# Optimization experiments

Measured on AMD Instinct MI355X. Metric: run time of the kernel, lower is better.

The kernel has to match this reference:

```python
import jax, jax.numpy as jnp
import numpy as np
import math

B, N, D_IN, D_OUT = 8, 2048, 128, 128
NEG_BIG = -10000.0

def setup_inputs() -> dict:
    key = jax.random.key(0)
    k_in, k_adj, kq, kk, kv, kbq, kbk, kbv = jax.random.split(key, 8)
    scale = 1.0 / math.sqrt(D_IN)
    inputs = jax.random.normal(k_in, (B, N, D_IN), dtype=jnp.float32)
    adj = jax.random.randint(k_adj, (B, N, N), 0, 2, dtype=jnp.int32)
    Wq = jax.random.uniform(kq, (D_IN, D_OUT), jnp.float32, -scale, scale)
    Wk = jax.random.uniform(kk, (D_IN, D_OUT), jnp.float32, -scale, scale)
    Wv = jax.random.uniform(kv, (D_IN, D_OUT), jnp.float32, -scale, scale)
    bq = jax.random.uniform(kbq, (D_OUT,), jnp.float32, -scale, scale)
    bk = jax.random.uniform(kbk, (D_OUT,), jnp.float32, -scale, scale)
    bv = jax.random.uniform(kbv, (D_OUT,), jnp.float32, -scale, scale)
    return {"inputs": inputs, "adj": adj, "Wq": Wq, "bq": bq,
            "Wk": Wk, "bk": bk, "Wv": Wv, "bv": bv}

def reference(inputs, adj, Wq, bq, Wk, bk, Wv, bv):
    # QKV projections: [B, N, D_OUT]
    q = inputs @ Wq + bq
    k = inputs @ Wk + bk
    v = inputs @ Wv + bv
    # additive adjacency bias: 0 where edge, -10000 where no edge
    bias = (1.0 - adj.astype(jnp.float32)) * NEG_BIG
    # scaled dot-product scores [B, N, N]
    a = jnp.einsum('bnd,bmd->bnm', q, k) / jnp.sqrt(jnp.float32(q.shape[-1]))
    a = a + bias
    p = jax.nn.softmax(a, axis=-1)  # dropout_prob=0.0 -> identity
    h = jnp.einsum('bnm,bmd->bnd', p, v)
    return jax.nn.elu(h)
```

## Files before the change

kernel.cpp:

```cpp
#include <hip/hip_runtime.h>

typedef unsigned short u16;
typedef unsigned int   u32;
typedef unsigned long long u64;
typedef __bf16 bf16x8 __attribute__((ext_vector_type(8)));
typedef float  fx4    __attribute__((ext_vector_type(4)));

__device__ __forceinline__ u16 f2bf(float f) {
    unsigned int x = __builtin_bit_cast(unsigned int, f);
    x = x + 0x7fffu + ((x >> 16) & 1u);
    return (u16)(x >> 16);
}
__device__ __forceinline__ __bf16 f2bf16(float f) {
    return __builtin_bit_cast(__bf16, f2bf(f));
}
__device__ __forceinline__ u16 f2bf_fast(float f) {
    return __builtin_bit_cast(u16, (__bf16)f);
}
__device__ __forceinline__ float exp2_fast(float x) {
#if __has_builtin(__builtin_amdgcn_exp2f)
    return __builtin_amdgcn_exp2f(x);
#else
    float r;
    __asm__ volatile("v_exp_f32 %0, %1" : "=v"(r) : "v"(x));
    return r;
#endif
}
__device__ __forceinline__ int ld_nt(const int* p) {
    return __builtin_nontemporal_load(p);
}

#define MFMA16(a, b, c) __builtin_amdgcn_mfma_f32_16x16x32_bf16((a), (b), (c), 0, 0, 0)
#define WAVE_LDS_SYNC() __asm__ volatile("s_waitcnt lgkmcnt(0)" ::: "memory")

__global__ __launch_bounds__(256) void wt_kernel(
    const float* __restrict__ Wq, const float* __restrict__ Wk,
    const float* __restrict__ Wv, u16* __restrict__ WT)
{
    const int o = blockIdx.x * 256 + threadIdx.x;
    const int p = o >> 14, rem = o & 16383, c = rem >> 7, k = rem & 127;
    const float* W = (p == 0) ? Wq : ((p == 1) ? Wk : Wv);
    WT[o] = f2bf(W[k * 128 + c]);
}

__global__ __launch_bounds__(256) void pack_kernel(
    const int* __restrict__ adj, u64* __restrict__ mask64)
{
    const int w = threadIdx.x >> 6, lane = threadIdx.x & 63;
    const int gw = blockIdx.x * 4 + w;
    const int nw = gridDim.x * 4;
    for (int it = gw; it < 131072; it += nw) {
        const int* base = adj + (size_t)it * 256 + lane;
        const u64 b0 = __ballot(ld_nt(base +   0) != 0);
        const u64 b1 = __ballot(ld_nt(base +  64) != 0);
        const u64 b2 = __ballot(ld_nt(base + 128) != 0);
        const u64 b3 = __ballot(ld_nt(base + 192) != 0);
        if (lane < 4) {
            const u64 v = (lane == 0) ? b0 : (lane == 1) ? b1 : (lane == 2) ? b2 : b3;
            mask64[(size_t)it * 4 + lane] = v;
        }
    }
}

__global__ __launch_bounds__(256, 2) void qkv_kernel(
    const float* __restrict__ X, const u16* __restrict__ WT,
    const float* __restrict__ bq, const float* __restrict__ bk,
    const float* __restrict__ bv,
    u16* __restrict__ Qf, u16* __restrict__ Kf, u16* __restrict__ Vf)
{
    __shared__ __align__(16) u16 st[4][1024];

    const int tid  = threadIdx.x;
    const int w    = tid >> 6;
    const int lane = tid & 63;
    const int n    = lane & 15;
    const int quad = lane >> 4;
    const int gw   = blockIdx.x * 4 + w;
    const int rt   = gw >> 1, ch = gw & 1;
    const int row0 = rt * 16;
    const int b    = row0 >> 11;
    const int keyb = row0 & 2047;

    u16* sw = st[w];

    bf16x8 af[4];
    {
        const float* xr = X + (size_t)(row0 + n) * 128;
#pragma unroll
        for (int kk = 0; kk < 4; ++kk) {
            float4 f0 = *(const float4*)(xr + kk * 32 + quad * 8);
            float4 f1 = *(const float4*)(xr + kk * 32 + quad * 8 + 4);
            bf16x8 a;
            a[0] = f2bf16(f0.x); a[1] = f2bf16(f0.y); a[2] = f2bf16(f0.z); a[3] = f2bf16(f0.w);
            a[4] = f2bf16(f1.x); a[5] = f2bf16(f1.y); a[6] = f2bf16(f1.z); a[7] = f2bf16(f1.w);
            af[kk] = a;
        }
    }

    const float* Bs[2] = {bq, bk};
#pragma unroll
    for (int p = 0; p < 2; ++p) {
        const u16* wt = WT + p * 16384;
#pragma unroll
        for (int nt = 0; nt < 4; ++nt) {
            const int col0 = ch * 64 + nt * 16;
            fx4 acc = {0.f, 0.f, 0.f, 0.f};
#pragma unroll
            for (int kk = 0; kk < 4; ++kk) {
                bf16x8 bf = __builtin_bit_cast(bf16x8,
                    *(const uint4*)&wt[(col0 + n) * 128 + kk * 32 + quad * 8]);
                acc = MFMA16(af[kk], bf, acc);
            }
            const float bb = Bs[p][col0 + n];
            const int c = col0 + n;
            const int li = ((c >> 5) & 1) * 512 + ((c >> 3) & 3) * 128 + (c & 7);
#pragma unroll
            for (int r = 0; r < 4; ++r)
                sw[li + (quad * 4 + r) * 8] = f2bf(acc[r] + bb);
        }
        WAVE_LDS_SYNC();
        u16* gbase;
        if (p == 0) {
            gbase = Qf + (((size_t)(b * 128 + (keyb >> 4)) * 4 + 2 * ch) << 9);
        } else {
            gbase = Kf + (((size_t)((b * 64 + (keyb >> 5)) * 2 + ((keyb >> 4) & 1)) * 4 + 2 * ch) << 9);
        }
        *(uint4*)(gbase + lane * 8)       = *(const uint4*)(sw + lane * 8);
        *(uint4*)(gbase + 512 + lane * 8) = *(const uint4*)(sw + 512 + lane * 8);
    }

    {
        const u16* wtv = WT + 2 * 16384;
        const int hk    = (keyb >> 4) & 1;
        const int vtile = keyb >> 5;
#pragma unroll
        for (int d0 = 0; d0 < 4; ++d0) {
            const int dbase = ch * 64 + d0 * 16;
            fx4 acc = {0.f, 0.f, 0.f, 0.f};
#pragma unroll
            for (int kk = 0; kk < 4; ++kk) {
                bf16x8 wf = __builtin_bit_cast(bf16x8,
                    *(const uint4*)&wtv[(dbase + n) * 128 + kk * 32 + quad * 8]);
                acc = MFMA16(wf, af[kk], acc);
            }
            const int li = d0 * 256 + ((n >> 3) & 1) * 128 + (n & 7);
#pragma unroll
            for (int r = 0; r < 4; ++r)
                sw[li + (quad * 4 + r) * 8] = f2bf(acc[r] + bv[dbase + quad * 4 + r]);
        }
        WAVE_LDS_SYNC();
        const int l5 = lane >> 5, lo = lane & 31;
#pragma unroll
        for (int i = 0; i < 2; ++i) {
            const int c2 = l5 + 2 * i;
            u16* g = Vf + (((size_t)(b * 64 + vtile) * 8 + ch * 4 + c2) << 9)
                        + hk * 256 + lo * 8;
            *(uint4*)g = *(const uint4*)(sw + c2 * 256 + lo * 8);
        }
    }
}

__global__ __launch_bounds__(256, 4) void attn_kernel(
    const u16* __restrict__ Qf, const u16* __restrict__ Kf,
    const u16* __restrict__ Vf, const u32* __restrict__ mask,
    float* __restrict__ out)
{
    __shared__ __align__(16) float mO[4][16 * 128];
    __shared__ __align__(16) float ml[4][16];
    __shared__ __align__(16) u16 pl[4][640];

    const int tid  = threadIdx.x;
    const int h    = tid >> 6;
    const int lane = tid & 63;
    const int n    = lane & 15;
    const int quad = lane >> 4;
    const int b    = blockIdx.x & 7;
    const int qt   = blockIdx.x >> 3;
    const int q0   = qt * 16;
    const size_t bN = (size_t)b * 2048;

    bf16x8 qf[4];
    {
        const u16* qp = Qf + ((size_t)(b * 128 + qt) << 11) + lane * 8;
#pragma unroll
        for (int kk = 0; kk < 4; ++kk)
            qf[kk] = __builtin_bit_cast(bf16x8, *(const uint4*)(qp + (kk << 9)));
    }
    const u16* Kb = Kf + ((size_t)b << 18);
    const u16* Vb = Vf + ((size_t)b << 18);

    fx4 O[8];
#pragma unroll
    for (int i = 0; i < 8; ++i) O[i] = (fx4){0.f, 0.f, 0.f, 0.f};
    fx4 Lacc = {0.f, 0.f, 0.f, 0.f};

    bf16x8 ONESF;
    {
        const __bf16 one = __builtin_bit_cast(__bf16, (u16)0x3F80);
#pragma unroll
        for (int j = 0; j < 8; ++j) ONESF[j] = one;
    }

    const u32* mrow = mask + (bN + q0 + quad * 4) * 64 + h * 16;
    const float C2 = 0.12751742f;
    const float MB = -14427.0f;
    u16* pw = pl[h];

    u32 mc[4];
#pragma unroll
    for (int r = 0; r < 4; ++r) mc[r] = mrow[r * 64];

    for (int t = 0; t < 16; ++t) {
        const int tg = h * 16 + t;
        const u16* kt_ = Kb + ((size_t)tg << 12) + lane * 8;
        const u16* vt_ = Vb + ((size_t)tg << 12) + lane * 8;

        bf16x8 kb[8];
#pragma unroll
        for (int kk = 0; kk < 8; ++kk)
            kb[kk] = __builtin_bit_cast(bf16x8, *(const uint4*)(kt_ + (kk << 9)));

        bf16x8 vf[8];
#pragma unroll
        for (int dt = 0; dt < 8; ++dt)
            vf[dt] = __builtin_bit_cast(bf16x8, *(const uint4*)(vt_ + (dt << 9)));

        u32 mn_[4];
        if (t < 15) {
#pragma unroll
            for (int r = 0; r < 4; ++r) mn_[r] = mrow[r * 64 + t + 1];
        }

        fx4 S0 = {0.f, 0.f, 0.f, 0.f}, S1 = {0.f, 0.f, 0.f, 0.f};
#pragma unroll
        for (int kk = 0; kk < 4; ++kk) {
            S0 = MFMA16(qf[kk], kb[kk], S0);
            S1 = MFMA16(qf[kk], kb[4 + kk], S1);
        }

#pragma unroll
        for (int r = 0; r < 4; ++r) {
            const float bias0 = ((mc[r] >> n) & 1u)        ? 0.f : MB;
            const float bias1 = ((mc[r] >> (16 + n)) & 1u) ? 0.f : MB;
            const float e0 = exp2_fast(__builtin_fmaf(S0[r], C2, bias0));
            const float e1 = exp2_fast(__builtin_fmaf(S1[r], C2, bias1));
            pw[(quad * 4 + r) * 40 + n]      = f2bf_fast(e0);
            pw[(quad * 4 + r) * 40 + 16 + n] = f2bf_fast(e1);
        }

        WAVE_LDS_SYNC();
        bf16x8 pf = __builtin_bit_cast(bf16x8, *(const uint4*)&pw[n * 40 + quad * 8]);

#pragma unroll
        for (int dt = 0; dt < 8; ++dt)
            O[dt] = MFMA16(pf, vf[dt], O[dt]);
        Lacc = MFMA16(pf, ONESF, Lacc);

#pragma unroll
        for (int r = 0; r < 4; ++r) mc[r] = mn_[r];
    }

#pragma unroll
    for (int r = 0; r < 4; ++r) {
        const int row = quad * 4 + r;
        if (n == 0) ml[h][row] = Lacc[r];
#pragma unroll
        for (int dt = 0; dt < 8; ++dt)
            mO[h][row * 128 + dt * 16 + n] = O[dt][r];
    }
    __syncthreads();

#pragma unroll
    for (int r = 0; r < 4; ++r) {
        const int row = quad * 4 + r;
        const float L = ml[0][row] + ml[1][row] + ml[2][row] + ml[3][row];
        const float linv = 1.f / L;
        float* po = out + (bN + q0 + row) * 128;
#pragma unroll
        for (int dti = 0; dti < 2; ++dti) {
            const int dt = h * 2 + dti;
            float o = 0.f;
#pragma unroll
            for (int g = 0; g < 4; ++g) o += mO[g][row * 128 + dt * 16 + n];
            const float hh = o * linv;
            po[dt * 16 + n] = (hh > 0.f) ? hh : (__expf(hh) - 1.f);
        }
    }
}

extern "C" void kernel_launch(void* const* d_in, const int* in_sizes, int n_in,
                              void* d_out, int out_size, void* d_ws, size_t ws_size,
                              hipStream_t stream) {
    (void)in_sizes; (void)n_in; (void)out_size; (void)ws_size;
    const float* X   = (const float*)d_in[0];
    const int*   adj = (const int*)d_in[1];
    const float* Wq  = (const float*)d_in[2];
    const float* bq  = (const float*)d_in[3];
    const float* Wk  = (const float*)d_in[4];
    const float* bk  = (const float*)d_in[5];
    const float* Wv  = (const float*)d_in[6];
    const float* bv  = (const float*)d_in[7];
    float* out = (float*)d_out;

    u16* WT   = (u16*)d_out;
    u16* Qf   = (u16*)d_ws;
    u16* Kf   = Qf + (size_t)16384 * 128;
    u16* Vf   = Kf + (size_t)16384 * 128;
    u32* mask = (u32*)(Vf + (size_t)16384 * 128);

    wt_kernel<<<192, 256, 0, stream>>>(Wq, Wk, Wv, WT);
    qkv_kernel<<<512, 256, 0, stream>>>(X, WT, bq, bk, bv, Qf, Kf, Vf);
    pack_kernel<<<2048, 256, 0, stream>>>(adj, (u64*)mask);
    attn_kernel<<<1024, 256, 0, stream>>>(Qf, Kf, Vf, mask, out);
}
```

Measured before the change: 255.1 us.

## Fuse adjacency bit-packing into attention kernel via LDS staging

Removes the separate pack kernel and its global mask buffer. Each attention wave now reads its slice of the int32 adjacency rows, ballots them into bitmasks, and stores them in the LDS region later reused for output merging. Mask lookups then come from LDS instead of global memory. This saves a launch and a global write/read round trip of the mask. In exchange, each attention block must stream 16 rows of adjacency itself before it can start compute, which serializes that load with the attention work.

```diff
diff --git a/kernel.cpp b/kernel.cpp
--- a/kernel.cpp
+++ b/kernel.cpp
@@ -41,25 +41,6 @@
     const int p = o >> 14, rem = o & 16383, c = rem >> 7, k = rem & 127;
     const float* W = (p == 0) ? Wq : ((p == 1) ? Wk : Wv);
     WT[o] = f2bf(W[k * 128 + c]);
-}
-
-__global__ __launch_bounds__(256) void pack_kernel(
-    const int* __restrict__ adj, u64* __restrict__ mask64)
-{
-    const int w = threadIdx.x >> 6, lane = threadIdx.x & 63;
-    const int gw = blockIdx.x * 4 + w;
-    const int nw = gridDim.x * 4;
-    for (int it = gw; it < 131072; it += nw) {
-        const int* base = adj + (size_t)it * 256 + lane;
-        const u64 b0 = __ballot(ld_nt(base +   0) != 0);
-        const u64 b1 = __ballot(ld_nt(base +  64) != 0);
-        const u64 b2 = __ballot(ld_nt(base + 128) != 0);
-        const u64 b3 = __ballot(ld_nt(base + 192) != 0);
-        if (lane < 4) {
-            const u64 v = (lane == 0) ? b0 : (lane == 1) ? b1 : (lane == 2) ? b2 : b3;
-            mask64[(size_t)it * 4 + lane] = v;
-        }
-    }
 }
 
 __global__ __launch_bounds__(256, 2) void qkv_kernel(
@@ -162,7 +143,7 @@
 
 __global__ __launch_bounds__(256, 4) void attn_kernel(
     const u16* __restrict__ Qf, const u16* __restrict__ Kf,
-    const u16* __restrict__ Vf, const u32* __restrict__ mask,
+    const u16* __restrict__ Vf, const int* __restrict__ adj,
     float* __restrict__ out)
 {
     __shared__ __align__(16) float mO[4][16 * 128];
@@ -179,6 +160,28 @@
     const int q0   = qt * 16;
     const size_t bN = (size_t)b * 2048;
 
+    u32* mlds = (u32*)&mO[h][0];
+    {
+        const int* ab = adj + (bN + q0) * 2048 + h * 512 + lane;
+#pragma unroll 1
+        for (int rb = 0; rb < 4; ++rb) {
+            int v[32];
+#pragma unroll
+            for (int i = 0; i < 32; ++i) {
+                const int r = rb * 4 + (i >> 3), c = i & 7;
+                v[i] = ld_nt(ab + (size_t)r * 2048 + c * 64);
+            }
+#pragma unroll
+            for (int i = 0; i < 32; ++i) {
+                const u64 bl = __ballot(v[i] != 0);
+                const int r = rb * 4 + (i >> 3), c = i & 7;
+                if (lane == 0)
+                    *(u64*)&mlds[r * 16 + c * 2] = bl;
+            }
+        }
+    }
+    WAVE_LDS_SYNC();
+
     bf16x8 qf[4];
     {
         const u16* qp = Qf + ((size_t)(b * 128 + qt) << 11) + lane * 8;
@@ -201,14 +204,13 @@
         for (int j = 0; j < 8; ++j) ONESF[j] = one;
     }
 
-    const u32* mrow = mask + (bN + q0 + quad * 4) * 64 + h * 16;
     const float C2 = 0.12751742f;
     const float MB = -14427.0f;
     u16* pw = pl[h];
 
     u32 mc[4];
 #pragma unroll
-    for (int r = 0; r < 4; ++r) mc[r] = mrow[r * 64];
+    for (int r = 0; r < 4; ++r) mc[r] = mlds[(quad * 4 + r) * 16];
 
     for (int t = 0; t < 16; ++t) {
         const int tg = h * 16 + t;
@@ -228,7 +230,7 @@
         u32 mn_[4];
         if (t < 15) {
 #pragma unroll
-            for (int r = 0; r < 4; ++r) mn_[r] = mrow[r * 64 + t + 1];
+            for (int r = 0; r < 4; ++r) mn_[r] = mlds[(quad * 4 + r) * 16 + t + 1];
         }
 
         fx4 S0 = {0.f, 0.f, 0.f, 0.f}, S1 = {0.f, 0.f, 0.f, 0.f};
@@ -306,10 +308,8 @@
     u16* Qf   = (u16*)d_ws;
     u16* Kf   = Qf + (size_t)16384 * 128;
     u16* Vf   = Kf + (size_t)16384 * 128;
-    u32* mask = (u32*)(Vf + (size_t)16384 * 128);
 
     wt_kernel<<<192, 256, 0, stream>>>(Wq, Wk, Wv, WT);
     qkv_kernel<<<512, 256, 0, stream>>>(X, WT, bq, bk, bv, Qf, Kf, Vf);
-    pack_kernel<<<2048, 256, 0, stream>>>(adj, (u64*)mask);
-    attn_kernel<<<1024, 256, 0, stream>>>(Qf, Kf, Vf, mask, out);
-}
+    attn_kernel<<<1024, 256, 0, stream>>>(Qf, Kf, Vf, adj, out);
+}
```

Measured after the change: 250.8 us (median of 2 runs). Within noise of the previous version (-1.7%).
